# Optimization experiments

Measured on AMD Instinct MI355X. Metric: run time of the kernel, lower is better.

## Reference

```python
import jax, jax.numpy as jnp
import numpy as np

E = 8      # num_experts
K = 2      # num_experts_per_tok
D = 1024   # n_embd
H = 1024   # expert_dim (= 2*n_embd // k)
B, T = 2, 1024


def setup_inputs() -> dict:
    key = jax.random.key(0)
    ks = jax.random.split(key, 6)
    s = 0.02  # weight init scale (keeps relu^2 activations tame)
    return {
        "x": jax.random.normal(ks[0], (B, T, D), dtype=jnp.float32),
        "gate_w": jax.random.normal(ks[1], (E, D), dtype=jnp.float32) * s,
        "lb_bias": jnp.zeros((E,), dtype=jnp.float32),
        "w1": jax.random.normal(ks[2], (E, H, D), dtype=jnp.float32) * s,
        "w2": jax.random.normal(ks[3], (E, D, H), dtype=jnp.float32) * s,
        "cfc": jax.random.normal(ks[4], (H, D), dtype=jnp.float32) * s,
        "cproj": jax.random.normal(ks[5], (D, H), dtype=jnp.float32) * s,
    }


def reference(x, gate_w, lb_bias, w1, w2, cfc, cproj):
    Bx, Tx, Dx = x.shape
    # --- Router: top-k over (logits + load-balance bias), sigmoid gating ---
    logits = jnp.einsum('btd,ed->bte', x, gate_w)               # (B,T,E)
    _, idx = jax.lax.top_k(logits + lb_bias, K)                  # (B,T,K)
    sel_logits = jnp.take_along_axis(logits, idx, axis=-1)       # (B,T,K)
    w = jax.nn.sigmoid(sel_logits)
    w = w / (jnp.sum(w, axis=-1, keepdims=True) + 1e-6)          # (B,T,K)

    # --- Dispatch/combine (dense-equivalent of the per-expert gather loop) ---
    xf = x.reshape(-1, Dx)                                       # (N,D)
    idxf = idx.reshape(-1, K)                                    # (N,K)
    wf = w.reshape(-1, K)                                        # (N,K)
    onehot = jax.nn.one_hot(idxf, E, dtype=wf.dtype)             # (N,K,E)
    we = jnp.einsum('nke,nk->ne', onehot, wf)                    # combined per-expert weight (N,E)

    hidden = jnp.square(jax.nn.relu(jnp.einsum('nd,ehd->neh', xf, w1)))  # (N,E,H)
    expert_out = jnp.einsum('neh,edh->ned', hidden, w2)                  # (N,E,D)
    moe_out = jnp.einsum('ned,ne->nd', expert_out, we).reshape(Bx, Tx, Dx)

    # --- Shared expert (always active): relu(x W1^T)^2 W2^T ---
    sh = jnp.square(jax.nn.relu(jnp.einsum('btd,hd->bth', x, cfc)))
    shared = jnp.einsum('bth,dh->btd', sh, cproj)
    return moe_out + shared
```

## Files before the change

### kernel.cpp

```cpp
#include <hip/hip_runtime.h>
#include <stdint.h>

#define D_DIM 1024
#define H_DIM 1024
#define NE 8
#define NTOK 2048
#define SB 5120
#define TOTAL_ROWS 7168
#define GEMM_BLKS 448
#define CONV2_BLKS 4608
#define M8 (8 * 1024 * 1024)

typedef __bf16 bf16;
typedef bf16 bf16x8 __attribute__((ext_vector_type(8)));
typedef float f32x4 __attribute__((ext_vector_type(4)));

#define GL16(SRC, DST)                                               \
  __builtin_amdgcn_global_load_lds(                                  \
      (const __attribute__((address_space(1))) void*)(SRC),          \
      (__attribute__((address_space(3))) void*)(DST), 16, 0, 0)

#define WS_NTILES     0
#define WS_TILE_E     64
#define WS_TILE_BASE  576
#define WS_EIDX       2048
#define WS_WTOK       18432
#define WS_TOK        34816
#define WS_SLOT       63488
#define WS_XG         131072
#define WS_HID        16777216
#define WS_W1B        33554432
#define WS_W2B        50331648
#define WS_CFCB       67108864
#define WS_CPROJB     69206016

__global__ __launch_bounds__(256) void convrouter(
    const float* __restrict__ x, const float* __restrict__ gw,
    const float* __restrict__ lb, int* __restrict__ eidx,
    float* __restrict__ wtok, bf16* __restrict__ xg,
    const float* __restrict__ w1, const float* __restrict__ cfc,
    bf16* __restrict__ w1b, bf16* __restrict__ cfcb) {
  const int bx = blockIdx.x;
  if (bx >= 512) {
    int i = ((bx - 512) * 256 + threadIdx.x) * 8;
    const float* s;
    bf16* d;
    if (i < M8) { s = w1 + i;        d = w1b + i; }
    else        { s = cfc + (i - M8); d = cfcb + (i - M8); }
    float4 a = *(const float4*)(s);
    float4 b = *(const float4*)(s + 4);
    union { uint4 v; bf16 h[8]; } t;
    t.h[0] = (bf16)a.x; t.h[1] = (bf16)a.y; t.h[2] = (bf16)a.z; t.h[3] = (bf16)a.w;
    t.h[4] = (bf16)b.x; t.h[5] = (bf16)b.y; t.h[6] = (bf16)b.z; t.h[7] = (bf16)b.w;
    *(uint4*)(d) = t.v;
    return;
  }
  const int wave = threadIdx.x >> 6;
  const int lane = threadIdx.x & 63;
  const int n = bx * 4 + wave;

  const float4* xr = (const float4*)(x + (size_t)n * D_DIM);
  float4 xv[4];
#pragma unroll
  for (int q = 0; q < 4; q++) xv[q] = xr[q * 64 + lane];

  float acc[NE];
#pragma unroll
  for (int e = 0; e < NE; e++) acc[e] = 0.f;
#pragma unroll
  for (int e = 0; e < NE; e++) {
    const float4* gr = (const float4*)(gw + e * D_DIM);
#pragma unroll
    for (int q = 0; q < 4; q++) {
      float4 g = gr[q * 64 + lane];
      acc[e] += xv[q].x * g.x + xv[q].y * g.y + xv[q].z * g.z + xv[q].w * g.w;
    }
  }

  bf16* dst = xg + (size_t)n * D_DIM;
#pragma unroll
  for (int q = 0; q < 4; q++) {
    union { ushort4 u; bf16 h[4]; } t;
    t.h[0] = (bf16)xv[q].x; t.h[1] = (bf16)xv[q].y;
    t.h[2] = (bf16)xv[q].z; t.h[3] = (bf16)xv[q].w;
    *(ushort4*)(dst + (q * 64 + lane) * 4) = t.u;
  }

#pragma unroll
  for (int e = 0; e < NE; e++)
#pragma unroll
    for (int off = 32; off > 0; off >>= 1) acc[e] += __shfl_xor(acc[e], off, 64);

  if (lane == 0) {
    float b[NE];
#pragma unroll
    for (int e = 0; e < NE; e++) b[e] = acc[e] + lb[e];
    int i0 = 0; float v0 = b[0];
#pragma unroll
    for (int e = 1; e < NE; e++) if (b[e] > v0) { v0 = b[e]; i0 = e; }
    int i1 = -1; float v1 = -3.4e38f;
#pragma unroll
    for (int e = 0; e < NE; e++) if (e != i0 && b[e] > v1) { v1 = b[e]; i1 = e; }
    float s0 = 1.f / (1.f + expf(-acc[i0]));
    float s1 = 1.f / (1.f + expf(-acc[i1]));
    float s = s0 + s1 + 1e-6f;
    eidx[n * 2] = i0;     wtok[n * 2] = s0 / s;
    eidx[n * 2 + 1] = i1; wtok[n * 2 + 1] = s1 / s;
  }
}

__global__ __launch_bounds__(256) void assign_kernel(
    const int* __restrict__ eidx, int* __restrict__ tE, int* __restrict__ tB,
    int* __restrict__ ntiles, int* __restrict__ tok,
    int* __restrict__ slotIdx) {
  __shared__ int segCnt[64][NE];
  __shared__ int segBase[64][NE];
  const int tid = threadIdx.x;
  const int wave = tid >> 6, lane = tid & 63;
  const unsigned long long below = (lane == 0) ? 0ull : ((~0ull) >> (64 - lane));

  int e16[16], pr16[16];
#pragma unroll
  for (int t = 0; t < 16; t++) {
    const int r = t * 256 + tid;
    const int seg = t * 4 + wave;
    const int e = eidx[r];
    int prior = 0;
#pragma unroll
    for (int ee = 0; ee < NE; ee++) {
      unsigned long long m = __ballot(e == ee);
      if (e == ee) prior = __popcll(m & below);
      if (lane == ee) segCnt[seg][ee] = __popcll(m);
    }
    e16[t] = e; pr16[t] = prior;
  }

  for (int s = tid; s < TOTAL_ROWS; s += 256) {
    tok[s] = (s < SB) ? 0 : (s - SB);
  }
  __syncthreads();

  if (wave == 0) {
    int v[NE], inc[NE];
#pragma unroll
    for (int e = 0; e < NE; e++) { v[e] = segCnt[lane][e]; inc[e] = v[e]; }
#pragma unroll
    for (int off = 1; off < 64; off <<= 1) {
#pragma unroll
      for (int e = 0; e < NE; e++) {
        int u = __shfl_up(inc[e], off);
        if (lane >= off) inc[e] += u;
      }
    }
    int tot[NE];
#pragma unroll
    for (int e = 0; e < NE; e++) tot[e] = __shfl(inc[e], 63);
    int offsL[NE]; int b = 0;
#pragma unroll
    for (int e = 0; e < NE; e++) { offsL[e] = b; b += ((tot[e] + 127) >> 7) << 7; }
#pragma unroll
    for (int e = 0; e < NE; e++) segBase[lane][e] = offsL[e] + (inc[e] - v[e]);
    if (lane == 0) {
      int nt = 0;
      for (int e = 0; e < NE; e++) {
        int t128 = (tot[e] + 127) >> 7;
        for (int t = 0; t < t128; t++) { tE[nt] = e; tB[nt] = offsL[e] + t * 128; nt++; }
      }
      for (int t = 0; t < 16; t++) { tE[nt] = NE; tB[nt] = SB + t * 128; nt++; }
      ntiles[0] = nt;
      ntiles[1] = nt;
    }
  }
  __syncthreads();

#pragma unroll
  for (int t = 0; t < 16; t++) {
    const int r = t * 256 + tid;
    const int seg = t * 4 + wave;
    const int slot = segBase[seg][e16[t]] + pr16[t];
    tok[slot] = r >> 1;
    slotIdx[r] = slot;
  }
}

template <int MODE>
__global__ __launch_bounds__(256) void moe_gemm(
    const bf16* __restrict__ Ab, const bf16* __restrict__ We,
    const bf16* __restrict__ Ws, const int* __restrict__ tE,
    const int* __restrict__ tB, const int* __restrict__ ntp,
    bf16* __restrict__ Cout, const int* __restrict__ tok,
    const float* __restrict__ cvs1, const float* __restrict__ cvs2,
    bf16* __restrict__ cvd1, bf16* __restrict__ cvd2) {
  if (MODE == 0 && blockIdx.x >= GEMM_BLKS) {
    int i = ((blockIdx.x - GEMM_BLKS) * 256 + threadIdx.x) * 8;
    const float* s;
    bf16* d;
    if (i < M8) { s = cvs1 + i;        d = cvd1 + i; }
    else        { s = cvs2 + (i - M8); d = cvd2 + (i - M8); }
    float4 a = *(const float4*)(s);
    float4 b = *(const float4*)(s + 4);
    union { uint4 v; bf16 h[8]; } t;
    t.h[0] = (bf16)a.x; t.h[1] = (bf16)a.y; t.h[2] = (bf16)a.z; t.h[3] = (bf16)a.w;
    t.h[4] = (bf16)b.x; t.h[5] = (bf16)b.y; t.h[6] = (bf16)b.z; t.h[7] = (bf16)b.w;
    *(uint4*)(d) = t.v;
    return;
  }

  const int per = ntp[1];
  const int g = blockIdx.x & 7, idx = blockIdx.x >> 3;
  if (idx >= per) return;
  const int p = g * per + idx;
  const int mslot = p >> 3;
  const int n0 = (p & 7) * 128;
  const int e = tE[mslot];
  const int base = tB[mslot];
  const bf16* Bp = (e < NE) ? (We + (size_t)e * (H_DIM * D_DIM)) : Ws;

  __shared__ bf16 As[2 * 4096];
  __shared__ bf16 Bs[2 * 4096];

  const int tid = threadIdx.x;
  const int wave = tid >> 6, lane = tid & 63;

  const int rS = tid >> 2, sS = tid & 3;
  const int cS = sS ^ ((rS >> 1) & 3);
  size_t rowA1, rowA2;
  if (MODE == 0) { rowA1 = tok[base + rS]; rowA2 = tok[base + 64 + rS]; }
  else           { rowA1 = base + rS;      rowA2 = base + 64 + rS; }
  const bf16* gA1 = Ab + rowA1 * 1024 + cS * 8;
  const bf16* gA2 = Ab + rowA2 * 1024 + cS * 8;
  const bf16* gB1 = Bp + (size_t)(n0 + rS) * 1024 + cS * 8;
  const bf16* gB2 = Bp + (size_t)(n0 + 64 + rS) * 1024 + cS * 8;
  bf16* laBase = As + tid * 8;
  bf16* lbBase = Bs + tid * 8;

  const int wm = (wave >> 1) * 64, wn = (wave & 1) * 64;
  const int fr = lane & 15, chk = lane >> 4;
  int aOff[4], bOff[4];
#pragma unroll
  for (int i = 0; i < 4; i++) {
    const int r = wm + i * 16 + fr;
    aOff[i] = r * 32 + ((chk ^ ((r >> 1) & 3)) * 8);
  }
#pragma unroll
  for (int j = 0; j < 4; j++) {
    const int r = wn + j * 16 + fr;
    bOff[j] = r * 32 + ((chk ^ ((r >> 1) & 3)) * 8);
  }

  const f32x4 zero = {0.f, 0.f, 0.f, 0.f};
  f32x4 acc[4][4];
#pragma unroll
  for (int i = 0; i < 4; i++)
#pragma unroll
    for (int j = 0; j < 4; j++) acc[i][j] = zero;

  GL16(gA1, laBase);
  GL16(gA2, laBase + 2048);
  GL16(gB1, lbBase);
  GL16(gB2, lbBase + 2048);

  for (int kt = 0; kt < 32; ++kt) {
    const int cur = kt & 1;
    __syncthreads();
    if (kt + 1 < 32) {
      const int koff = (kt + 1) * 32;
      const int bo = (cur ^ 1) * 4096;
      GL16(gA1 + koff, laBase + bo);
      GL16(gA2 + koff, laBase + bo + 2048);
      GL16(gB1 + koff, lbBase + bo);
      GL16(gB2 + koff, lbBase + bo + 2048);
    }
    bf16x8 af[4], bv[4];
#pragma unroll
    for (int i = 0; i < 4; i++) af[i] = *(const bf16x8*)&As[cur * 4096 + aOff[i]];
#pragma unroll
    for (int j = 0; j < 4; j++) bv[j] = *(const bf16x8*)&Bs[cur * 4096 + bOff[j]];
#pragma unroll
    for (int i = 0; i < 4; i++)
#pragma unroll
      for (int j = 0; j < 4; j++)
        acc[i][j] = __builtin_amdgcn_mfma_f32_16x16x32_bf16(af[i], bv[j],
                                                            acc[i][j], 0, 0, 0);
  }

  const int rbase = (lane >> 4) * 4;
#pragma unroll
  for (int i = 0; i < 4; i++) {
#pragma unroll
    for (int j = 0; j < 4; j++) {
      const int col = n0 + wn + j * 16 + fr;
#pragma unroll
      for (int r = 0; r < 4; r++) {
        const int orow = wm + i * 16 + rbase + r;
        float v = acc[i][j][r];
        if (MODE == 0) v = v > 0.f ? v * v : 0.f;
        Cout[(size_t)(base + orow) * 1024 + col] = (bf16)v;
      }
    }
  }
}

__global__ __launch_bounds__(256) void combine_kernel(
    const bf16* __restrict__ eo, const int* __restrict__ slotIdx,
    const float* __restrict__ wtok, float* __restrict__ out) {
  const int t = blockIdx.x;
  const int c = threadIdx.x * 4;
  const int s0 = slotIdx[t * 2], s1 = slotIdx[t * 2 + 1];
  const float w0 = wtok[t * 2], w1 = wtok[t * 2 + 1];
  union U { uint2 v; bf16 h[4]; };
  U a, b, sh;
  a.v  = *(const uint2*)(eo + (size_t)s0 * 1024 + c);
  b.v  = *(const uint2*)(eo + (size_t)s1 * 1024 + c);
  sh.v = *(const uint2*)(eo + (size_t)(SB + t) * 1024 + c);
  float4 o;
  o.x = w0 * (float)a.h[0] + w1 * (float)b.h[0] + (float)sh.h[0];
  o.y = w0 * (float)a.h[1] + w1 * (float)b.h[1] + (float)sh.h[1];
  o.z = w0 * (float)a.h[2] + w1 * (float)b.h[2] + (float)sh.h[2];
  o.w = w0 * (float)a.h[3] + w1 * (float)b.h[3] + (float)sh.h[3];
  *(float4*)(out + (size_t)t * 1024 + c) = o;
}

extern "C" void kernel_launch(void* const* d_in, const int* in_sizes, int n_in,
                              void* d_out, int out_size, void* d_ws,
                              size_t ws_size, hipStream_t stream) {
  const float* x     = (const float*)d_in[0];
  const float* gw    = (const float*)d_in[1];
  const float* lb    = (const float*)d_in[2];
  const float* w1    = (const float*)d_in[3];
  const float* w2    = (const float*)d_in[4];
  const float* cfc   = (const float*)d_in[5];
  const float* cproj = (const float*)d_in[6];
  float* out = (float*)d_out;
  char* ws = (char*)d_ws;

  int*   ntl   = (int*)(ws + WS_NTILES);
  int*   tE    = (int*)(ws + WS_TILE_E);
  int*   tB    = (int*)(ws + WS_TILE_BASE);
  int*   eidx  = (int*)(ws + WS_EIDX);
  float* wtok  = (float*)(ws + WS_WTOK);
  int*   tok   = (int*)(ws + WS_TOK);
  int*   slotI = (int*)(ws + WS_SLOT);
  bf16*  xg    = (bf16*)(ws + WS_XG);
  bf16*  hid   = (bf16*)(ws + WS_HID);
  bf16*  w1b   = (bf16*)(ws + WS_W1B);
  bf16*  w2b   = (bf16*)(ws + WS_W2B);
  bf16*  cfcb  = (bf16*)(ws + WS_CFCB);
  bf16*  cprojb= (bf16*)(ws + WS_CPROJB);

  convrouter<<<5120, 256, 0, stream>>>(x, gw, lb, eidx, wtok, xg,
                                       w1, cfc, w1b, cfcb);
  assign_kernel<<<1, 256, 0, stream>>>(eidx, tE, tB, ntl, tok, slotI);

  moe_gemm<0><<<GEMM_BLKS + CONV2_BLKS, 256, 0, stream>>>(
      xg, w1b, cfcb, tE, tB, ntl, hid, tok, w2, cproj, w2b, cprojb);
  moe_gemm<1><<<GEMM_BLKS, 256, 0, stream>>>(
      hid, w2b, cprojb, tE, tB, ntl, xg, tok, nullptr, nullptr, nullptr, nullptr);
  combine_kernel<<<NTOK, 256, 0, stream>>>(xg, slotI, wtok, out);
}
```

Measured before the change: 98.18 us.

## Triple-buffer GEMM K-loop with explicit vmcnt waits and MFMA priority

Replaces the double-buffered K loop with a three-stage LDS ring. Three tiles are prefetched up front, and each iteration waits only for the oldest tile using explicit `s_waitcnt vmcnt` counts. A second barrier after the LDS fragment reads lets the next global-to-LDS load reuse the just-consumed buffer. MFMA issue is wrapped in `s_setprio`, so memory latency has more iterations to hide behind compute. The cost is LDS growing from 32KB to 48KB per block, which may lower occupancy, plus an extra barrier per iteration.

```diff
diff --git a/kernel.cpp b/kernel.cpp
--- a/kernel.cpp
+++ b/kernel.cpp
@@ -216,8 +216,8 @@
   const int base = tB[mslot];
   const bf16* Bp = (e < NE) ? (We + (size_t)e * (H_DIM * D_DIM)) : Ws;
 
-  __shared__ bf16 As[2 * 4096];
-  __shared__ bf16 Bs[2 * 4096];
+  __shared__ bf16 As[3 * 4096];
+  __shared__ bf16 Bs[3 * 4096];
 
   const int tid = threadIdx.x;
   const int wave = tid >> 6, lane = tid & 63;
@@ -255,34 +255,51 @@
 #pragma unroll
     for (int j = 0; j < 4; j++) acc[i][j] = zero;
 
-  GL16(gA1, laBase);
-  GL16(gA2, laBase + 2048);
-  GL16(gB1, lbBase);
-  GL16(gB2, lbBase + 2048);
-
-  for (int kt = 0; kt < 32; ++kt) {
-    const int cur = kt & 1;
-    __syncthreads();
-    if (kt + 1 < 32) {
-      const int koff = (kt + 1) * 32;
-      const int bo = (cur ^ 1) * 4096;
-      GL16(gA1 + koff, laBase + bo);
-      GL16(gA2 + koff, laBase + bo + 2048);
-      GL16(gB1 + koff, lbBase + bo);
-      GL16(gB2 + koff, lbBase + bo + 2048);
-    }
-    bf16x8 af[4], bv[4];
-#pragma unroll
-    for (int i = 0; i < 4; i++) af[i] = *(const bf16x8*)&As[cur * 4096 + aOff[i]];
-#pragma unroll
-    for (int j = 0; j < 4; j++) bv[j] = *(const bf16x8*)&Bs[cur * 4096 + bOff[j]];
-#pragma unroll
-    for (int i = 0; i < 4; i++)
-#pragma unroll
-      for (int j = 0; j < 4; j++)
-        acc[i][j] = __builtin_amdgcn_mfma_f32_16x16x32_bf16(af[i], bv[j],
-                                                            acc[i][j], 0, 0, 0);
-  }
+#pragma unroll
+  for (int t = 0; t < 3; ++t) {
+    const int ko = t * 32;
+    const int bo = t * 4096;
+    GL16(gA1 + ko, laBase + bo);
+    GL16(gA2 + ko, laBase + bo + 2048);
+    GL16(gB1 + ko, lbBase + bo);
+    GL16(gB2 + ko, lbBase + bo + 2048);
+  }
+
+  int cur = 0;
+#define GEMM_ITER(KT, VMSTR, ISSUE)                                           \
+  {                                                                           \
+    asm volatile("s_waitcnt vmcnt(" VMSTR ")" ::: "memory");                  \
+    __builtin_amdgcn_s_barrier();              \
+    __builtin_amdgcn_sched_barrier(0);                                        \
+    bf16x8 af[4], bv[4];                                                      \
+    _Pragma("unroll") for (int i = 0; i < 4; i++)                             \
+        af[i] = *(const bf16x8*)&As[cur * 4096 + aOff[i]];                    \
+    _Pragma("unroll") for (int j = 0; j < 4; j++)                             \
+        bv[j] = *(const bf16x8*)&Bs[cur * 4096 + bOff[j]];                    \
+    asm volatile("s_waitcnt lgkmcnt(0)" ::: "memory");                        \
+    __builtin_amdgcn_s_barrier();             \
+    __builtin_amdgcn_sched_barrier(0);                                        \
+    if (ISSUE) {                                                              \
+      const int ko = ((KT) + 3) * 32;                                         \
+      const int bo = cur * 4096;                                              \
+      GL16(gA1 + ko, laBase + bo);                                            \
+      GL16(gA2 + ko, laBase + bo + 2048);                                     \
+      GL16(gB1 + ko, lbBase + bo);                                            \
+      GL16(gB2 + ko, lbBase + bo + 2048);                                     \
+    }                                                                         \
+    __builtin_amdgcn_s_setprio(1);                                            \
+    _Pragma("unroll") for (int i = 0; i < 4; i++)                             \
+      _Pragma("unroll") for (int j = 0; j < 4; j++)                           \
+          acc[i][j] = __builtin_amdgcn_mfma_f32_16x16x32_bf16(                \
+              af[i], bv[j], acc[i][j], 0, 0, 0);                              \
+    __builtin_amdgcn_s_setprio(0);                                            \
+    cur = (cur == 2) ? 0 : cur + 1;                                           \
+  }
+
+  for (int kt = 0; kt < 30; ++kt) GEMM_ITER(kt, "8", (kt < 29));
+  GEMM_ITER(30, "4", false);
+  GEMM_ITER(31, "0", false);
+#undef GEMM_ITER
 
   const int rbase = (lane >> 4) * 4;
 #pragma unroll
```

New measurement: 82.93 us. 1.18x faster.
